# Kernel optimization log

Measured on AMD Instinct MI355X. Metric: run time of the kernel, lower is better.

The kernel has to match this reference:

```python
import jax, jax.numpy as jnp
import numpy as np

D = 2048      # hidden
H = 16        # heads
HD = 128      # head dim
E = 64        # experts
K = 8         # top-k
F = 1024      # expert intermediate
B, S = 1, 256
EPS = 1e-05
THETA = 10000.0
SCALE = 0.08838834764831845  # 1/sqrt(128)


def _rms(x, w):
    return x * jax.lax.rsqrt(jnp.mean(x * x, axis=-1, keepdims=True) + EPS) * w


def _rotate_half(x):
    h = x.shape[-1] // 2
    return jnp.concatenate([-x[..., h:], x[..., :h]], axis=-1)


def setup_inputs() -> dict:
    key = jax.random.key(0)
    ks = jax.random.split(key, 16)
    std = 0.02
    return {
        "x": jax.random.normal(ks[0], (B, S, D), jnp.float32),
        "ln1_w": jnp.ones((D,), jnp.float32),
        "q_w": jax.random.normal(ks[1], (D, D), jnp.float32) * std,
        "k_w": jax.random.normal(ks[2], (D, D), jnp.float32) * std,
        "v_w": jax.random.normal(ks[3], (D, D), jnp.float32) * std,
        "o_w": jax.random.normal(ks[4], (D, D), jnp.float32) * std,
        "qn_w": jnp.ones((D,), jnp.float32),
        "kn_w": jnp.ones((D,), jnp.float32),
        "ln2_w": jnp.ones((D,), jnp.float32),
        "router_w": jax.random.normal(ks[5], (E, D), jnp.float32) * std,
        "gate_w": jax.random.normal(ks[6], (E, F, D), jnp.float32) * std,
        "up_w": jax.random.normal(ks[7], (E, F, D), jnp.float32) * std,
        "down_w": jax.random.normal(ks[8], (E, D, F), jnp.float32) * std,
    }


def reference(x, ln1_w, q_w, k_w, v_w, o_w, qn_w, kn_w, ln2_w,
              router_w, gate_w, up_w, down_w):
    b, s, d = x.shape
    # ---- attention ----
    xn = _rms(x, ln1_w)
    q = _rms(jnp.einsum('bsd,od->bso', xn, q_w), qn_w)
    k = _rms(jnp.einsum('bsd,od->bso', xn, k_w), kn_w)
    v = jnp.einsum('bsd,od->bso', xn, v_w)
    q = q.reshape(b, s, H, HD).transpose(0, 2, 1, 3)  # [b,h,s,hd]
    k = k.reshape(b, s, H, HD).transpose(0, 2, 1, 3)
    v = v.reshape(b, s, H, HD).transpose(0, 2, 1, 3)
    # RoPE
    inv_freq = 1.0 / (THETA ** (jnp.arange(0, HD, 2, dtype=jnp.float32) / HD))
    ang = jnp.arange(s, dtype=jnp.float32)[:, None] * inv_freq[None, :]  # [s, hd/2]
    emb = jnp.concatenate([ang, ang], axis=-1)
    cos, sin = jnp.cos(emb).astype(x.dtype), jnp.sin(emb).astype(x.dtype)
    q = q * cos + _rotate_half(q) * sin
    k = k * cos + _rotate_half(k) * sin
    scores = jnp.einsum('bhqd,bhkd->bhqk', q, k) * SCALE
    causal = jnp.tril(jnp.ones((s, s), bool))
    scores = jnp.where(causal, scores, jnp.finfo(scores.dtype).min)
    attn = jax.nn.softmax(scores, axis=-1)
    ctx = jnp.einsum('bhqk,bhkd->bhqd', attn, v)
    ctx = ctx.transpose(0, 2, 1, 3).reshape(b, s, d)
    h = x + jnp.einsum('bsd,od->bso', ctx, o_w)
    # ---- MoE ----
    hn = _rms(h, ln2_w)
    logits = jnp.einsum('bsd,ed->bse', hn, router_w)
    probs = jax.nn.softmax(logits.astype(jnp.float32), axis=-1)
    vals, idx = jax.lax.top_k(probs, K)  # [b,s,K]
    # dense combine weights [b,s,E]; OLMoE does not renormalize top-k probs
    combine = jnp.sum(jax.nn.one_hot(idx, E, dtype=jnp.float32) * vals[..., None], axis=-2)
    combine = combine.reshape(-1, E).astype(x.dtype)  # [T,E]
    xf = hn.reshape(-1, d)                            # [T,D]
    g = jnp.einsum('td,efd->etf', xf, gate_w)         # [E,T,F]
    u = jnp.einsum('td,efd->etf', xf, up_w)
    mid = jax.nn.silu(g) * u
    eo = jnp.einsum('etf,edf->etd', mid, down_w)      # [E,T,D]
    y = jnp.einsum('te,etd->td', combine, eo).reshape(b, s, d)
    return h + y
```

## Files before the change

kernel.cpp:

```cpp
#include <hip/hip_runtime.h>
#include <math.h>

#define DHID 2048
#define TOK 256
#define NHEAD 16
#define HDIM 128
#define NEXP 64
#define KSEL 8
#define FFD 1024
#define RMSEPS 1e-5f
#define ATTNSCALE 0.08838834764831845f

typedef short bf16x8 __attribute__((ext_vector_type(8)));
typedef float f32x4 __attribute__((ext_vector_type(4)));

__device__ __forceinline__ float bf2f(unsigned short u){
  union { unsigned int u; float f; } c; c.u = ((unsigned int)u)<<16; return c.f;
}
__device__ __forceinline__ unsigned short f2bf(float f){
  union { float f; unsigned int u; } c; c.f = f;
  unsigned int u = c.u + 0x7fffu + ((c.u>>16)&1u);
  return (unsigned short)(u>>16);
}
__device__ __forceinline__ unsigned int pk2(float a, float b){
  return (unsigned int)f2bf(a) | ((unsigned int)f2bf(b)<<16);
}
__device__ __forceinline__ bf16x8 as_bf8(uint4 u){
  union { uint4 u; bf16x8 v; } c; c.u = u; return c.v;
}

#define WAITV(N) { asm volatile("s_waitcnt vmcnt(" #N ")" ::: "memory"); __builtin_amdgcn_sched_barrier(0); }
#define WAITL0   { asm volatile("s_waitcnt lgkmcnt(0)" ::: "memory"); __builtin_amdgcn_sched_barrier(0); }
#define SB       __builtin_amdgcn_sched_barrier(0);

__global__ __launch_bounds__(256) void rms_kernel(const float* __restrict__ x,
    const float* __restrict__ w, unsigned short* __restrict__ obf,
    float* __restrict__ of32)
{
  int row = blockIdx.x, tid = threadIdx.x;
  const float* xr = x + (size_t)row*DHID;
  float4 a = *(const float4*)(xr + tid*8);
  float4 b = *(const float4*)(xr + tid*8 + 4);
  float ss = a.x*a.x+a.y*a.y+a.z*a.z+a.w*a.w + b.x*b.x+b.y*b.y+b.z*b.z+b.w*b.w;
  #pragma unroll
  for(int o=32;o>0;o>>=1) ss += __shfl_down(ss,o);
  __shared__ float red[4];
  if((tid&63)==0) red[tid>>6]=ss;
  __syncthreads();
  float r = rsqrtf((red[0]+red[1]+red[2]+red[3])*(1.0f/DHID) + RMSEPS);
  float v[8] = {a.x,a.y,a.z,a.w,b.x,b.y,b.z,b.w};
  unsigned short ob[8];
  #pragma unroll
  for(int j=0;j<8;j++){
    float val = v[j]*r*w[tid*8+j];
    ob[j]=f2bf(val);
    if(of32) of32[(size_t)row*DHID + tid*8 + j] = val;
  }
  uint4 o4;
  o4.x = (unsigned int)ob[0] | ((unsigned int)ob[1]<<16);
  o4.y = (unsigned int)ob[2] | ((unsigned int)ob[3]<<16);
  o4.z = (unsigned int)ob[4] | ((unsigned int)ob[5]<<16);
  o4.w = (unsigned int)ob[6] | ((unsigned int)ob[7]<<16);
  *(uint4*)(obf + (size_t)row*DHID + tid*8) = o4;
}

__global__ void rope_table_kernel(float* __restrict__ cs, float* __restrict__ sn){
  int i = blockIdx.x*256 + threadIdx.x;
  int s = i>>6, j = i&63;
  float invf = powf(10000.0f, -(float)j*(1.0f/64.0f));
  float ang = (float)s * invf;
  cs[i] = cosf(ang); sn[i] = sinf(ang);
}

__global__ __launch_bounds__(256) void gemm_qkv_kernel(
    const unsigned short* __restrict__ A,
    const float* __restrict__ qw, const float* __restrict__ kw, const float* __restrict__ vw,
    float* __restrict__ qo, float* __restrict__ ko, float* __restrict__ vo)
{
  int nt = blockIdx.x, mt = blockIdx.y;
  int which = nt>>5, nb = nt&31;
  const float* W = (which==0)? qw : (which==1)? kw : vw;
  float* OUT = (which==0)? qo : (which==1)? ko : vo;
  int n0 = nb*64, m0 = mt*64;
  __shared__ unsigned short As[64*64];
  __shared__ unsigned short Bs[64*64];
  int tid = threadIdx.x;
  int wid = tid>>6, lane = tid&63;
  int wm = wid>>1, wn = wid&1;
  int lr = lane&15, lg = lane>>4;
  int sr = tid>>2, sq = tid&3;
  f32x4 acc[2][2] = {};
  const unsigned short* Ap = A + (size_t)(m0+sr)*DHID + sq*16;
  const float* Bp = W + (size_t)(n0+sr)*DHID + sq*16;
  for(int k0=0;k0<DHID;k0+=64){
    uint4 a0 = *(const uint4*)(Ap + k0);
    uint4 a1 = *(const uint4*)(Ap + k0 + 8);
    float4 b0 = *(const float4*)(Bp + k0);
    float4 b1 = *(const float4*)(Bp + k0 + 4);
    float4 b2 = *(const float4*)(Bp + k0 + 8);
    float4 b3 = *(const float4*)(Bp + k0 + 12);
    int x7 = sr&7;
    *(uint4*)&As[sr*64 + (((sq*2)  ^ x7)*8)] = a0;
    *(uint4*)&As[sr*64 + (((sq*2+1)^ x7)*8)] = a1;
    uint4 p0 = make_uint4(pk2(b0.x,b0.y),pk2(b0.z,b0.w),pk2(b1.x,b1.y),pk2(b1.z,b1.w));
    uint4 p1 = make_uint4(pk2(b2.x,b2.y),pk2(b2.z,b2.w),pk2(b3.x,b3.y),pk2(b3.z,b3.w));
    *(uint4*)&Bs[sr*64 + (((sq*2)  ^ x7)*8)] = p0;
    *(uint4*)&Bs[sr*64 + (((sq*2+1)^ x7)*8)] = p1;
    __syncthreads();
    #pragma unroll
    for(int ki=0;ki<2;ki++){
      bf16x8 af[2], bfr[2];
      #pragma unroll
      for(int mi=0;mi<2;mi++){
        int r = wm*32 + mi*16 + lr;
        af[mi] = *(const bf16x8*)&As[r*64 + (((ki*4+lg)^(r&7))*8)];
      }
      #pragma unroll
      for(int ni=0;ni<2;ni++){
        int r = wn*32 + ni*16 + lr;
        bfr[ni] = *(const bf16x8*)&Bs[r*64 + (((ki*4+lg)^(r&7))*8)];
      }
      #pragma unroll
      for(int mi=0;mi<2;mi++)
        #pragma unroll
        for(int ni=0;ni<2;ni++)
          acc[mi][ni] = __builtin_amdgcn_mfma_f32_16x16x32_bf16(af[mi], bfr[ni], acc[mi][ni], 0,0,0);
    }
    __syncthreads();
  }
  #pragma unroll
  for(int mi=0;mi<2;mi++){
    #pragma unroll
    for(int ni=0;ni<2;ni++){
      int col = n0 + wn*32 + ni*16 + lr;
      int rowb = m0 + wm*32 + mi*16 + lg*4;
      #pragma unroll
      for(int rg=0;rg<4;rg++)
        OUT[(size_t)(rowb+rg)*DHID + col] = acc[mi][ni][rg];
    }
  }
}

__global__ __launch_bounds__(256) void gemm_o_kernel(const float* __restrict__ A,
  const float* __restrict__ W, const float* __restrict__ X,
  float* __restrict__ H, float* __restrict__ O)
{
  int nb = blockIdx.x, mt = blockIdx.y;
  int n0 = nb*64, m0 = mt*64;
  __shared__ unsigned short As[64*64];
  __shared__ unsigned short Bs[64*64];
  int tid = threadIdx.x;
  int wid = tid>>6, lane = tid&63;
  int wm = wid>>1, wn = wid&1;
  int lr = lane&15, lg = lane>>4;
  int sr = tid>>2, sq = tid&3;
  f32x4 acc[2][2] = {};
  const float* Ap = A + (size_t)(m0+sr)*DHID + sq*16;
  const float* Bp = W + (size_t)(n0+sr)*DHID + sq*16;
  for(int k0=0;k0<DHID;k0+=64){
    float4 a0=*(const float4*)(Ap+k0),   a1=*(const float4*)(Ap+k0+4);
    float4 a2=*(const float4*)(Ap+k0+8), a3=*(const float4*)(Ap+k0+12);
    float4 b0=*(const float4*)(Bp+k0),   b1=*(const float4*)(Bp+k0+4);
    float4 b2=*(const float4*)(Bp+k0+8), b3=*(const float4*)(Bp+k0+12);
    int x7 = sr&7;
    uint4 pa0 = make_uint4(pk2(a0.x,a0.y),pk2(a0.z,a0.w),pk2(a1.x,a1.y),pk2(a1.z,a1.w));
    uint4 pa1 = make_uint4(pk2(a2.x,a2.y),pk2(a2.z,a2.w),pk2(a3.x,a3.y),pk2(a3.z,a3.w));
    uint4 pb0 = make_uint4(pk2(b0.x,b0.y),pk2(b0.z,b0.w),pk2(b1.x,b1.y),pk2(b1.z,b1.w));
    uint4 pb1 = make_uint4(pk2(b2.x,b2.y),pk2(b2.z,b2.w),pk2(b3.x,b3.y),pk2(b3.z,b3.w));
    *(uint4*)&As[sr*64 + (((sq*2)  ^ x7)*8)] = pa0;
    *(uint4*)&As[sr*64 + (((sq*2+1)^ x7)*8)] = pa1;
    *(uint4*)&Bs[sr*64 + (((sq*2)  ^ x7)*8)] = pb0;
    *(uint4*)&Bs[sr*64 + (((sq*2+1)^ x7)*8)] = pb1;
    __syncthreads();
    #pragma unroll
    for(int ki=0;ki<2;ki++){
      bf16x8 af[2], bfr[2];
      #pragma unroll
      for(int mi=0;mi<2;mi++){
        int r = wm*32 + mi*16 + lr;
        af[mi] = *(const bf16x8*)&As[r*64 + (((ki*4+lg)^(r&7))*8)];
      }
      #pragma unroll
      for(int ni=0;ni<2;ni++){
        int r = wn*32 + ni*16 + lr;
        bfr[ni] = *(const bf16x8*)&Bs[r*64 + (((ki*4+lg)^(r&7))*8)];
      }
      #pragma unroll
      for(int mi=0;mi<2;mi++)
        #pragma unroll
        for(int ni=0;ni<2;ni++)
          acc[mi][ni] = __builtin_amdgcn_mfma_f32_16x16x32_bf16(af[mi], bfr[ni], acc[mi][ni], 0,0,0);
    }
    __syncthreads();
  }
  #pragma unroll
  for(int mi=0;mi<2;mi++){
    #pragma unroll
    for(int ni=0;ni<2;ni++){
      int col = n0 + wn*32 + ni*16 + lr;
      int rowb = m0 + wm*32 + mi*16 + lg*4;
      #pragma unroll
      for(int rg=0;rg<4;rg++){
        size_t idx = (size_t)(rowb+rg)*DHID + col;
        float v = acc[mi][ni][rg] + X[idx];
        H[idx] = v; O[idx] = v;
      }
    }
  }
}

__global__ __launch_bounds__(256) void qknorm_rope_kernel(const float* __restrict__ in,
   const float* __restrict__ w, const float* __restrict__ cs, const float* __restrict__ sn,
   float* __restrict__ out)
{
  int t = blockIdx.x, tid = threadIdx.x;
  __shared__ float xs[DHID];
  const float* xr = in + (size_t)t*DHID;
  float4 a = *(const float4*)(xr + tid*8);
  float4 b = *(const float4*)(xr + tid*8 + 4);
  *(float4*)&xs[tid*8] = a; *(float4*)&xs[tid*8+4] = b;
  float ss = a.x*a.x+a.y*a.y+a.z*a.z+a.w*a.w + b.x*b.x+b.y*b.y+b.z*b.z+b.w*b.w;
  #pragma unroll
  for(int o=32;o>0;o>>=1) ss += __shfl_down(ss,o);
  __shared__ float red[4];
  if((tid&63)==0) red[tid>>6]=ss;
  __syncthreads();
  float r = rsqrtf((red[0]+red[1]+red[2]+red[3])*(1.0f/DHID) + RMSEPS);
  int hh = tid>>4, jb = (tid&15)*4;
  #pragma unroll
  for(int p=0;p<4;p++){
    int j = jb+p;
    int i0 = hh*HDIM + j, i1 = i0+64;
    float va = xs[i0]*r*w[i0];
    float vb = xs[i1]*r*w[i1];
    float c = cs[t*64+j], s = sn[t*64+j];
    out[((size_t)(hh*TOK + t))*HDIM + j]    = va*c - vb*s;
    out[((size_t)(hh*TOK + t))*HDIM + j+64] = vb*c + va*s;
  }
}

__global__ __launch_bounds__(256) void vreshape_kernel(const float* __restrict__ v,
    float* __restrict__ vh)
{
  int t = blockIdx.x, tid = threadIdx.x;
  int i = tid*8;
  int hh = i>>7, d0 = i&127;
  float4 a = *(const float4*)(v + (size_t)t*DHID + i);
  float4 b = *(const float4*)(v + (size_t)t*DHID + i + 4);
  *(float4*)(vh + ((size_t)(hh*TOK+t))*HDIM + d0)     = a;
  *(float4*)(vh + ((size_t)(hh*TOK+t))*HDIM + d0 + 4) = b;
}

__global__ __launch_bounds__(256) void attn_kernel(const float* __restrict__ qh,
  const float* __restrict__ kh, const float* __restrict__ vh, float* __restrict__ ctx)
{
  int head = blockIdx.x>>4, qt = blockIdx.x&15;
  __shared__ float qs[16][132];
  __shared__ float sc[16][260];
  __shared__ float red[16][16];
  __shared__ float rmx[16], rsm[16];
  int tid = threadIdx.x;
  {
    int r = tid>>4, c = (tid&15)*8;
    const float* src = qh + ((size_t)(head*TOK + qt*16 + r))*HDIM + c;
    *(float4*)&qs[r][c]   = *(const float4*)(src);
    *(float4*)&qs[r][c+4] = *(const float4*)(src+4);
  }
  __syncthreads();
  int qi = tid&15, kk = tid>>4;
  int qg = qt*16 + qi;
  for(int k=kk; k<=qg; k+=16){
    const float* kp = kh + ((size_t)(head*TOK + k))*HDIM;
    float d = 0.f;
    #pragma unroll 8
    for(int c=0;c<128;c+=4){
      float4 kv = *(const float4*)(kp + c);
      float4 qv = *(const float4*)&qs[qi][c];
      d += qv.x*kv.x + qv.y*kv.y + qv.z*kv.z + qv.w*kv.w;
    }
    sc[qi][k] = d*ATTNSCALE;
  }
  float m = -1e30f;
  for(int k=kk;k<=qg;k+=16) m = fmaxf(m, sc[qi][k]);
  red[qi][kk] = m;
  __syncthreads();
  if(kk==0){
    float mm=-1e30f;
    #pragma unroll
    for(int j=0;j<16;j++) mm = fmaxf(mm, red[qi][j]);
    rmx[qi]=mm;
  }
  __syncthreads();
  float mm = rmx[qi];
  float s = 0.f;
  for(int k=kk;k<=qg;k+=16){ float pp = expf(sc[qi][k]-mm); sc[qi][k]=pp; s+=pp; }
  red[qi][kk]=s;
  __syncthreads();
  if(kk==0){
    float t_=0.f;
    #pragma unroll
    for(int j=0;j<16;j++) t_ += red[qi][j];
    rsm[qi]=t_;
  }
  __syncthreads();
  int dg = kk;
  float acc[8]={0,0,0,0,0,0,0,0};
  const float* vp = vh + (size_t)head*TOK*HDIM + dg*8;
  for(int k=0;k<=qg;k++){
    float p = sc[qi][k];
    float4 v0 = *(const float4*)(vp + (size_t)k*HDIM);
    float4 v1 = *(const float4*)(vp + (size_t)k*HDIM + 4);
    acc[0]+=p*v0.x; acc[1]+=p*v0.y; acc[2]+=p*v0.z; acc[3]+=p*v0.w;
    acc[4]+=p*v1.x; acc[5]+=p*v1.y; acc[6]+=p*v1.z; acc[7]+=p*v1.w;
  }
  float inv = 1.0f/rsm[qi];
  float* op = ctx + ((size_t)(qt*16+qi))*DHID + head*HDIM + dg*8;
  *(float4*)(op)   = make_float4(acc[0]*inv, acc[1]*inv, acc[2]*inv, acc[3]*inv);
  *(float4*)(op+4) = make_float4(acc[4]*inv, acc[5]*inv, acc[6]*inv, acc[7]*inv);
}

__global__ __launch_bounds__(256) void router_kernel(const float* __restrict__ hn,
    const float* __restrict__ rw, int* __restrict__ counts, int* __restrict__ toklist,
    float* __restrict__ wlist)
{
  int t = blockIdx.x, tid = threadIdx.x;
  __shared__ float xs[DHID];
  __shared__ float part[NEXP*4];
  __shared__ float probs[NEXP];
  *(float4*)&xs[tid*8]   = *(const float4*)(hn + (size_t)t*DHID + tid*8);
  *(float4*)&xs[tid*8+4] = *(const float4*)(hn + (size_t)t*DHID + tid*8+4);
  __syncthreads();
  int e = tid&63, c = tid>>6;
  const float* w = rw + (size_t)e*DHID + c*512;
  const float* xc = xs + c*512;
  float d = 0.f;
  for(int i=0;i<512;i+=4){
    float4 wv = *(const float4*)(w+i);
    d += xc[i]*wv.x + xc[i+1]*wv.y + xc[i+2]*wv.z + xc[i+3]*wv.w;
  }
  part[c*64 + e] = d;
  __syncthreads();
  if(tid<64){
    float logit = part[tid] + part[64+tid] + part[128+tid] + part[192+tid];
    float m = logit;
    #pragma unroll
    for(int o=32;o>0;o>>=1) m = fmaxf(m, __shfl_xor(m,o));
    float p = expf(logit - m);
    float s = p;
    #pragma unroll
    for(int o=32;o>0;o>>=1) s += __shfl_xor(s,o);
    probs[tid] = p/s;
  }
  __syncthreads();
  if(tid==0){
    unsigned long long used = 0ull;
    for(int r=0;r<KSEL;r++){
      float best = -1.f; int bi = 0;
      for(int j=0;j<NEXP;j++){
        if(!((used>>j)&1ull) && probs[j]>best){ best=probs[j]; bi=j; }
      }
      used |= (1ull<<bi);
      int slot = atomicAdd(&counts[bi],1);
      toklist[bi*TOK+slot] = t;
      wlist[bi*TOK+slot] = best;
    }
  }
}

__global__ void scan_kernel(const int* __restrict__ counts, int* __restrict__ offs){
  int e = threadIdx.x;
  int c = counts[e];
  int v = c;
  #pragma unroll
  for(int o=1;o<64;o<<=1){
    int n = __shfl_up(v,o);
    if(e>=o) v += n;
  }
  offs[e] = v - c;
}

__global__ __launch_bounds__(256,4) void moe_gateup_kernel(const unsigned short* __restrict__ hnb,
  const float* __restrict__ gw, const float* __restrict__ uw,
  const int* __restrict__ counts, const int* __restrict__ offs,
  const int* __restrict__ toklist, const float* __restrict__ wlist,
  unsigned short* __restrict__ mid)
{
  int fb = blockIdx.x, e = blockIdx.y, mc = blockIdx.z;
  int cnt = counts[e];
  if(mc*32 >= cnt) return;
  int base = offs[e];
  __shared__ unsigned short Gs[64*64];
  __shared__ unsigned short Us[64*64];
  int tid = threadIdx.x, w = tid>>6, lane = tid&63;
  int wm = w>>1, wn = w&1, lr = lane&15, lg = lane>>4;
  int sr = tid>>2, sq = tid&3, x7 = sr&7;

  const float* Gp = gw + ((size_t)e*FFD + fb*64 + sr)*DHID + sq*16;
  const float* Up = uw + ((size_t)e*FFD + fb*64 + sr)*DHID + sq*16;
  int aslot = mc*32 + wm*16 + lr;
  int acl = (aslot<cnt)? aslot : (cnt-1);
  const unsigned short* Ap = hnb + (size_t)toklist[e*TOK+acl]*DHID + lg*8;

  f32x4 ag[2]={}, au[2]={};
  float4 A_g0,A_g1,A_g2,A_g3, A_u0,A_u1,A_u2,A_u3;
  float4 B_g0,B_g1,B_g2,B_g3, B_u0,B_u1,B_u2,B_u3;
  uint4  A_a0,A_a1, B_a0,B_a1;

  #define GU_ISSUE_W(P,k0) { \
    P##g0=*(const float4*)(Gp+(k0));    P##g1=*(const float4*)(Gp+(k0)+4); \
    P##g2=*(const float4*)(Gp+(k0)+8);  P##g3=*(const float4*)(Gp+(k0)+12); \
    P##u0=*(const float4*)(Up+(k0));    P##u1=*(const float4*)(Up+(k0)+4); \
    P##u2=*(const float4*)(Up+(k0)+8);  P##u3=*(const float4*)(Up+(k0)+12); }
  #define GU_ISSUE_A(P,k0) { \
    P##a0=*(const uint4*)(Ap+(k0)); P##a1=*(const uint4*)(Ap+(k0)+32); }
  #define GU_WRITE(P) { \
    uint4 q0=make_uint4(pk2(P##g0.x,P##g0.y),pk2(P##g0.z,P##g0.w),pk2(P##g1.x,P##g1.y),pk2(P##g1.z,P##g1.w)); \
    uint4 q1=make_uint4(pk2(P##g2.x,P##g2.y),pk2(P##g2.z,P##g2.w),pk2(P##g3.x,P##g3.y),pk2(P##g3.z,P##g3.w)); \
    uint4 q2=make_uint4(pk2(P##u0.x,P##u0.y),pk2(P##u0.z,P##u0.w),pk2(P##u1.x,P##u1.y),pk2(P##u1.z,P##u1.w)); \
    uint4 q3=make_uint4(pk2(P##u2.x,P##u2.y),pk2(P##u2.z,P##u2.w),pk2(P##u3.x,P##u3.y),pk2(P##u3.z,P##u3.w)); \
    *(uint4*)&Gs[sr*64 + (((sq*2)  ^x7)*8)] = q0; \
    *(uint4*)&Gs[sr*64 + (((sq*2+1)^x7)*8)] = q1; \
    *(uint4*)&Us[sr*64 + (((sq*2)  ^x7)*8)] = q2; \
    *(uint4*)&Us[sr*64 + (((sq*2+1)^x7)*8)] = q3; }
  #define GU_COMPUTE(P) { \
    bf16x8 af0=as_bf8(P##a0), af1=as_bf8(P##a1); \
    _Pragma("unroll") \
    for(int ni=0;ni<2;ni++){ \
      int R = wn*32 + ni*16 + lr; \
      _Pragma("unroll") \
      for(int ki=0;ki<2;ki++){ \
        int off = R*64 + (((ki*4+lg)^(R&7))*8); \
        bf16x8 gfr = *(const bf16x8*)&Gs[off]; \
        bf16x8 ufr = *(const bf16x8*)&Us[off]; \
        bf16x8 afk = ki ? af1 : af0; \
        ag[ni] = __builtin_amdgcn_mfma_f32_16x16x32_bf16(afk, gfr, ag[ni], 0,0,0); \
        au[ni] = __builtin_amdgcn_mfma_f32_16x16x32_bf16(afk, ufr, au[ni], 0,0,0); \
      } \
    } }

  const int NT = DHID/64;
  GU_ISSUE_W(A_,0)   GU_ISSUE_A(A_,0)
  GU_ISSUE_W(B_,64)  GU_ISSUE_A(B_,64)

  for(int t=0;t<NT;t+=2){
    WAITV(10)
    GU_WRITE(A_)
    if(t+2<NT){ GU_ISSUE_W(A_,(t+2)*64) }
    WAITL0
    __builtin_amdgcn_s_barrier(); SB
    GU_COMPUTE(A_)
    if(t+2<NT){ GU_ISSUE_A(A_,(t+2)*64) }
    __builtin_amdgcn_s_barrier(); SB
    if(t+3<NT){ WAITV(10) } else { WAITV(0) }
    GU_WRITE(B_)
    if(t+3<NT){ GU_ISSUE_W(B_,(t+3)*64) }
    WAITL0
    __builtin_amdgcn_s_barrier(); SB
    GU_COMPUTE(B_)
    if(t+3<NT){ GU_ISSUE_A(B_,(t+3)*64) }
    __builtin_amdgcn_s_barrier(); SB
  }
  #undef GU_ISSUE_W
  #undef GU_ISSUE_A
  #undef GU_WRITE
  #undef GU_COMPUTE

  #pragma unroll
  for(int ni=0;ni<2;ni++){
    int f = fb*64 + wn*32 + ni*16 + lr;
    #pragma unroll
    for(int rg=0;rg<4;rg++){
      int sl = wm*16 + lg*4 + rg;
      int slot = mc*32 + sl;
      if(slot < cnt){
        float cw = wlist[e*TOK + slot];
        float g = ag[ni][rg], u = au[ni][rg];
        float mval = g/(1.0f+expf(-g))*u*cw;
        mid[((size_t)(base+slot))*FFD + f] = f2bf(mval);
      }
    }
  }
}

__global__ __launch_bounds__(256,4) void moe_down_kernel(const unsigned short* __restrict__ mid,
  const float* __restrict__ dwn, const int* __restrict__ counts, const int* __restrict__ offs,
  const int* __restrict__ toklist, float* __restrict__ out)
{
  int nb=blockIdx.x, e=blockIdx.y, mc=blockIdx.z;
  int cnt=counts[e];
  if(mc*32>=cnt) return;
  int base=offs[e];
  __shared__ unsigned short Ds[64*64];
  int tid=threadIdx.x, w=tid>>6, lane=tid&63;
  int wm=w>>1, wn=w&1, lr=lane&15, lg=lane>>4;
  int sr=tid>>2, sq=tid&3, x7=sr&7;

  const float* Dp = dwn + ((size_t)e*DHID + nb*64 + sr)*FFD + sq*16;
  int slot0 = mc*32 + wm*16 + lr;
  int sla = (slot0<cnt)? slot0 : (cnt-1);
  const unsigned short* Ap = mid + (size_t)(base+sla)*FFD + lg*8;

  f32x4 acc[2]={};
  float4 A_d0,A_d1,A_d2,A_d3, B_d0,B_d1,B_d2,B_d3;
  uint4  A_a0,A_a1, B_a0,B_a1;

  #define D_ISSUE_W(P,k0) { \
    P##d0=*(const float4*)(Dp+(k0));    P##d1=*(const float4*)(Dp+(k0)+4); \
    P##d2=*(const float4*)(Dp+(k0)+8);  P##d3=*(const float4*)(Dp+(k0)+12); }
  #define D_ISSUE_A(P,k0) { \
    P##a0=*(const uint4*)(Ap+(k0)); P##a1=*(const uint4*)(Ap+(k0)+32); }
  #define D_WRITE(P) { \
    uint4 q0=make_uint4(pk2(P##d0.x,P##d0.y),pk2(P##d0.z,P##d0.w),pk2(P##d1.x,P##d1.y),pk2(P##d1.z,P##d1.w)); \
    uint4 q1=make_uint4(pk2(P##d2.x,P##d2.y),pk2(P##d2.z,P##d2.w),pk2(P##d3.x,P##d3.y),pk2(P##d3.z,P##d3.w)); \
    *(uint4*)&Ds[sr*64 + (((sq*2)  ^x7)*8)] = q0; \
    *(uint4*)&Ds[sr*64 + (((sq*2+1)^x7)*8)] = q1; }
  #define D_COMPUTE(P) { \
    bf16x8 af0=as_bf8(P##a0), af1=as_bf8(P##a1); \
    _Pragma("unroll") \
    for(int ni=0;ni<2;ni++){ \
      int R = wn*32 + ni*16 + lr; \
      _Pragma("unroll") \
      for(int ki=0;ki<2;ki++){ \
        int off = R*64 + (((ki*4+lg)^(R&7))*8); \
        bf16x8 dfr = *(const bf16x8*)&Ds[off]; \
        bf16x8 afk = ki ? af1 : af0; \
        acc[ni] = __builtin_amdgcn_mfma_f32_16x16x32_bf16(afk, dfr, acc[ni], 0,0,0); \
      } \
    } }

  const int NT = FFD/64;
  D_ISSUE_W(A_,0)   D_ISSUE_A(A_,0)
  D_ISSUE_W(B_,64)  D_ISSUE_A(B_,64)

  for(int t=0;t<NT;t+=2){
    WAITV(6)
    D_WRITE(A_)
    if(t+2<NT){ D_ISSUE_W(A_,(t+2)*64) }
    WAITL0
    __builtin_amdgcn_s_barrier(); SB
    D_COMPUTE(A_)
    if(t+2<NT){ D_ISSUE_A(A_,(t+2)*64) }
    __builtin_amdgcn_s_barrier(); SB
    if(t+3<NT){ WAITV(6) } else { WAITV(0) }
    D_WRITE(B_)
    if(t+3<NT){ D_ISSUE_W(B_,(t+3)*64) }
    WAITL0
    __builtin_amdgcn_s_barrier(); SB
    D_COMPUTE(B_)
    if(t+3<NT){ D_ISSUE_A(B_,(t+3)*64) }
    __builtin_amdgcn_s_barrier(); SB
  }
  #undef D_ISSUE_W
  #undef D_ISSUE_A
  #undef D_WRITE
  #undef D_COMPUTE

  #pragma unroll
  for(int ni=0;ni<2;ni++){
    int d = nb*64 + wn*32 + ni*16 + lr;
    #pragma unroll
    for(int rg=0;rg<4;rg++){
      int sl=wm*16+lg*4+rg, slot=mc*32+sl;
      if(slot<cnt){
        int tok = toklist[e*TOK + slot];
        atomicAdd(out + (size_t)tok*DHID + d, acc[ni][rg]);
      }
    }
  }
}

extern "C" void kernel_launch(void* const* d_in, const int* in_sizes, int n_in,
                              void* d_out, int out_size, void* d_ws, size_t ws_size,
                              hipStream_t stream)
{
  (void)in_sizes; (void)n_in; (void)out_size; (void)ws_size;
  const float* x    = (const float*)d_in[0];
  const float* ln1w = (const float*)d_in[1];
  const float* qw   = (const float*)d_in[2];
  const float* kw   = (const float*)d_in[3];
  const float* vw   = (const float*)d_in[4];
  const float* ow   = (const float*)d_in[5];
  const float* qnw  = (const float*)d_in[6];
  const float* knw  = (const float*)d_in[7];
  const float* ln2w = (const float*)d_in[8];
  const float* rw   = (const float*)d_in[9];
  const float* gw   = (const float*)d_in[10];
  const float* uw   = (const float*)d_in[11];
  const float* dwn  = (const float*)d_in[12];
  float* out = (float*)d_out;

  char* p = (char*)d_ws;
  auto alloc = [&](size_t bytes)->void*{ void* r = (void*)p; p += (bytes + 255) & ~(size_t)255; return r; };
  unsigned short* xnb = (unsigned short*)alloc((size_t)TOK*DHID*2);
  float* qf   = (float*)alloc((size_t)TOK*DHID*4);
  float* kf   = (float*)alloc((size_t)TOK*DHID*4);
  float* vf   = (float*)alloc((size_t)TOK*DHID*4);
  float* qh   = (float*)alloc((size_t)TOK*DHID*4);
  float* kh   = (float*)alloc((size_t)TOK*DHID*4);
  float* vh   = (float*)alloc((size_t)TOK*DHID*4);
  float* ctx  = (float*)alloc((size_t)TOK*DHID*4);
  float* hbuf = (float*)alloc((size_t)TOK*DHID*4);
  float* hnf  = (float*)alloc((size_t)TOK*DHID*4);
  unsigned short* hnb = (unsigned short*)alloc((size_t)TOK*DHID*2);
  float* csb  = (float*)alloc((size_t)TOK*64*4);
  float* snb  = (float*)alloc((size_t)TOK*64*4);
  int* counts = (int*)alloc(NEXP*4);
  int* offs   = (int*)alloc(NEXP*4);
  int* toklist= (int*)alloc((size_t)NEXP*TOK*4);
  float* wlist= (float*)alloc((size_t)NEXP*TOK*4);
  unsigned short* mid = (unsigned short*)alloc((size_t)TOK*KSEL*FFD*2);

  rope_table_kernel<<<64,256,0,stream>>>(csb,snb);
  rms_kernel<<<TOK,256,0,stream>>>(x, ln1w, xnb, nullptr);
  gemm_qkv_kernel<<<dim3(96,4),256,0,stream>>>(xnb,qw,kw,vw,qf,kf,vf);
  qknorm_rope_kernel<<<TOK,256,0,stream>>>(qf,qnw,csb,snb,qh);
  qknorm_rope_kernel<<<TOK,256,0,stream>>>(kf,knw,csb,snb,kh);
  vreshape_kernel<<<TOK,256,0,stream>>>(vf,vh);
  attn_kernel<<<256,256,0,stream>>>(qh,kh,vh,ctx);
  gemm_o_kernel<<<dim3(32,4),256,0,stream>>>(ctx,ow,x,hbuf,out);
  rms_kernel<<<TOK,256,0,stream>>>(hbuf, ln2w, hnb, hnf);
  hipMemsetAsync(counts,0,NEXP*4,stream);
  router_kernel<<<TOK,256,0,stream>>>(hnf,rw,counts,toklist,wlist);
  scan_kernel<<<1,64,0,stream>>>(counts,offs);
  moe_gateup_kernel<<<dim3(16,NEXP,8),256,0,stream>>>(hnb,gw,uw,counts,offs,toklist,wlist,mid);
  moe_down_kernel<<<dim3(32,NEXP,8),256,0,stream>>>(mid,dwn,counts,offs,toklist,out);
}
```

Baseline: 707.5 us.

## Widen MoE K-tiles to 256 with coalesced weight loads; drop V reshape kernel

The MoE gate/up and down kernels now stage 256-wide K slices of the fp32 expert weights into LDS per step instead of 64-wide ones. Each thread issues eight strided float4 loads per half-tile, so adjacent lanes read adjacent 16-byte chunks and coalescing improves. Barriers per K step are also fewer. The cost is a much larger LDS footprint and register count, and launch bounds drop to 2 and 3 blocks per CU, so occupancy falls. Separately, the attention kernel reads V directly from the token-major projection output, which removes the vreshape kernel launch and its copy.

Result: faster. 642.2 us (-9.2%).

```diff
diff --git a/kernel.cpp b/kernel.cpp
--- a/kernel.cpp
+++ b/kernel.cpp
@@ -14,9 +14,6 @@
 typedef short bf16x8 __attribute__((ext_vector_type(8)));
 typedef float f32x4 __attribute__((ext_vector_type(4)));
 
-__device__ __forceinline__ float bf2f(unsigned short u){
-  union { unsigned int u; float f; } c; c.u = ((unsigned int)u)<<16; return c.f;
-}
 __device__ __forceinline__ unsigned short f2bf(float f){
   union { float f; unsigned int u; } c; c.f = f;
   unsigned int u = c.u + 0x7fffu + ((c.u>>16)&1u);
@@ -239,20 +236,8 @@
   }
 }
 
-__global__ __launch_bounds__(256) void vreshape_kernel(const float* __restrict__ v,
-    float* __restrict__ vh)
-{
-  int t = blockIdx.x, tid = threadIdx.x;
-  int i = tid*8;
-  int hh = i>>7, d0 = i&127;
-  float4 a = *(const float4*)(v + (size_t)t*DHID + i);
-  float4 b = *(const float4*)(v + (size_t)t*DHID + i + 4);
-  *(float4*)(vh + ((size_t)(hh*TOK+t))*HDIM + d0)     = a;
-  *(float4*)(vh + ((size_t)(hh*TOK+t))*HDIM + d0 + 4) = b;
-}
-
 __global__ __launch_bounds__(256) void attn_kernel(const float* __restrict__ qh,
-  const float* __restrict__ kh, const float* __restrict__ vh, float* __restrict__ ctx)
+  const float* __restrict__ kh, const float* __restrict__ vf, float* __restrict__ ctx)
 {
   int head = blockIdx.x>>4, qt = blockIdx.x&15;
   __shared__ float qs[16][132];
@@ -305,11 +290,11 @@
   __syncthreads();
   int dg = kk;
   float acc[8]={0,0,0,0,0,0,0,0};
-  const float* vp = vh + (size_t)head*TOK*HDIM + dg*8;
+  const float* vp = vf + head*HDIM + dg*8;
   for(int k=0;k<=qg;k++){
     float p = sc[qi][k];
-    float4 v0 = *(const float4*)(vp + (size_t)k*HDIM);
-    float4 v1 = *(const float4*)(vp + (size_t)k*HDIM + 4);
+    float4 v0 = *(const float4*)(vp + (size_t)k*DHID);
+    float4 v1 = *(const float4*)(vp + (size_t)k*DHID + 4);
     acc[0]+=p*v0.x; acc[1]+=p*v0.y; acc[2]+=p*v0.z; acc[3]+=p*v0.w;
     acc[4]+=p*v1.x; acc[5]+=p*v1.y; acc[6]+=p*v1.z; acc[7]+=p*v1.w;
   }
@@ -379,7 +364,7 @@
   offs[e] = v - c;
 }
 
-__global__ __launch_bounds__(256,4) void moe_gateup_kernel(const unsigned short* __restrict__ hnb,
+__global__ __launch_bounds__(256,2) void moe_gateup_kernel(const unsigned short* __restrict__ hnb,
   const float* __restrict__ gw, const float* __restrict__ uw,
   const int* __restrict__ counts, const int* __restrict__ offs,
   const int* __restrict__ toklist, const float* __restrict__ wlist,
@@ -389,81 +374,80 @@
   int cnt = counts[e];
   if(mc*32 >= cnt) return;
   int base = offs[e];
-  __shared__ unsigned short Gs[64*64];
-  __shared__ unsigned short Us[64*64];
+  __shared__ unsigned short Gs[64*256];
+  __shared__ unsigned short Us[64*256];
   int tid = threadIdx.x, w = tid>>6, lane = tid&63;
   int wm = w>>1, wn = w&1, lr = lane&15, lg = lane>>4;
-  int sr = tid>>2, sq = tid&3, x7 = sr&7;
-
-  const float* Gp = gw + ((size_t)e*FFD + fb*64 + sr)*DHID + sq*16;
-  const float* Up = uw + ((size_t)e*FFD + fb*64 + sr)*DHID + sq*16;
+  int srow = tid>>2, sc4 = tid&3, rx = srow&7;
+  int halfo = (sc4&1)*4, vbase = sc4>>1;
+
+  const float* Gp = gw + ((size_t)e*FFD + fb*64 + srow)*DHID + sc4*4;
+  const float* Up = uw + ((size_t)e*FFD + fb*64 + srow)*DHID + sc4*4;
   int aslot = mc*32 + wm*16 + lr;
   int acl = (aslot<cnt)? aslot : (cnt-1);
   const unsigned short* Ap = hnb + (size_t)toklist[e*TOK+acl]*DHID + lg*8;
 
   f32x4 ag[2]={}, au[2]={};
-  float4 A_g0,A_g1,A_g2,A_g3, A_u0,A_u1,A_u2,A_u3;
-  float4 B_g0,B_g1,B_g2,B_g3, B_u0,B_u1,B_u2,B_u3;
-  uint4  A_a0,A_a1, B_a0,B_a1;
-
-  #define GU_ISSUE_W(P,k0) { \
-    P##g0=*(const float4*)(Gp+(k0));    P##g1=*(const float4*)(Gp+(k0)+4); \
-    P##g2=*(const float4*)(Gp+(k0)+8);  P##g3=*(const float4*)(Gp+(k0)+12); \
-    P##u0=*(const float4*)(Up+(k0));    P##u1=*(const float4*)(Up+(k0)+4); \
-    P##u2=*(const float4*)(Up+(k0)+8);  P##u3=*(const float4*)(Up+(k0)+12); }
-  #define GU_ISSUE_A(P,k0) { \
-    P##a0=*(const uint4*)(Ap+(k0)); P##a1=*(const uint4*)(Ap+(k0)+32); }
-  #define GU_WRITE(P) { \
-    uint4 q0=make_uint4(pk2(P##g0.x,P##g0.y),pk2(P##g0.z,P##g0.w),pk2(P##g1.x,P##g1.y),pk2(P##g1.z,P##g1.w)); \
-    uint4 q1=make_uint4(pk2(P##g2.x,P##g2.y),pk2(P##g2.z,P##g2.w),pk2(P##g3.x,P##g3.y),pk2(P##g3.z,P##g3.w)); \
-    uint4 q2=make_uint4(pk2(P##u0.x,P##u0.y),pk2(P##u0.z,P##u0.w),pk2(P##u1.x,P##u1.y),pk2(P##u1.z,P##u1.w)); \
-    uint4 q3=make_uint4(pk2(P##u2.x,P##u2.y),pk2(P##u2.z,P##u2.w),pk2(P##u3.x,P##u3.y),pk2(P##u3.z,P##u3.w)); \
-    *(uint4*)&Gs[sr*64 + (((sq*2)  ^x7)*8)] = q0; \
-    *(uint4*)&Gs[sr*64 + (((sq*2+1)^x7)*8)] = q1; \
-    *(uint4*)&Us[sr*64 + (((sq*2)  ^x7)*8)] = q2; \
-    *(uint4*)&Us[sr*64 + (((sq*2+1)^x7)*8)] = q3; }
-  #define GU_COMPUTE(P) { \
-    bf16x8 af0=as_bf8(P##a0), af1=as_bf8(P##a1); \
-    _Pragma("unroll") \
-    for(int ni=0;ni<2;ni++){ \
-      int R = wn*32 + ni*16 + lr; \
+  float4 P[8], Q[8];
+  uint4 av[8];
+
+  #define ISSUE(BK,SRC,s,jb) { \
+    _Pragma("unroll") \
+    for(int j=0;j<8;j++) BK[j] = *(const float4*)(SRC + (s)*256 + ((jb)+j)*16); }
+  #define WRITE(BK,DST,jb) { \
+    _Pragma("unroll") \
+    for(int j=0;j<8;j++){ \
+      int v = ((jb)+j)*2 + vbase; \
+      int vp = (v & ~7) | ((v&7) ^ rx); \
+      uint2 val; val.x = pk2(BK[j].x,BK[j].y); val.y = pk2(BK[j].z,BK[j].w); \
+      *(uint2*)&DST[srow*256 + vp*8 + halfo] = val; } }
+  #define ISSUE_A(s) { \
+    _Pragma("unroll") \
+    for(int kf=0;kf<8;kf++) av[kf] = *(const uint4*)(Ap + (s)*256 + kf*32); }
+  #define COMPUTE() { \
+    _Pragma("unroll") \
+    for(int kf=0;kf<8;kf++){ \
+      bf16x8 af = as_bf8(av[kf]); \
       _Pragma("unroll") \
-      for(int ki=0;ki<2;ki++){ \
-        int off = R*64 + (((ki*4+lg)^(R&7))*8); \
-        bf16x8 gfr = *(const bf16x8*)&Gs[off]; \
-        bf16x8 ufr = *(const bf16x8*)&Us[off]; \
-        bf16x8 afk = ki ? af1 : af0; \
-        ag[ni] = __builtin_amdgcn_mfma_f32_16x16x32_bf16(afk, gfr, ag[ni], 0,0,0); \
-        au[ni] = __builtin_amdgcn_mfma_f32_16x16x32_bf16(afk, ufr, au[ni], 0,0,0); \
+      for(int ni=0;ni<2;ni++){ \
+        int R = wn*32 + ni*16 + lr; \
+        int v = kf*4 + lg; \
+        int vp = (v & ~7) | ((v&7) ^ (lr&7)); \
+        int ho = R*256 + vp*8; \
+        bf16x8 gfr = *(const bf16x8*)&Gs[ho]; \
+        bf16x8 ufr = *(const bf16x8*)&Us[ho]; \
+        ag[ni] = __builtin_amdgcn_mfma_f32_16x16x32_bf16(af, gfr, ag[ni], 0,0,0); \
+        au[ni] = __builtin_amdgcn_mfma_f32_16x16x32_bf16(af, ufr, au[ni], 0,0,0); \
       } \
     } }
 
-  const int NT = DHID/64;
-  GU_ISSUE_W(A_,0)   GU_ISSUE_A(A_,0)
-  GU_ISSUE_W(B_,64)  GU_ISSUE_A(B_,64)
-
-  for(int t=0;t<NT;t+=2){
-    WAITV(10)
-    GU_WRITE(A_)
-    if(t+2<NT){ GU_ISSUE_W(A_,(t+2)*64) }
+  const int NS = DHID/256;
+  ISSUE(P, Gp, 0, 0)
+  ISSUE(Q, Gp, 0, 8)
+  for(int s=0;s<NS;s++){
+    WAITV(8)
+    WRITE(P, Gs, 0)
+    ISSUE(P, Up, s, 0)
+    WAITV(8)
+    WRITE(Q, Gs, 8)
+    ISSUE(Q, Up, s, 8)
+    WAITV(8)
+    WRITE(P, Us, 0)
+    ISSUE_A(s)
+    WAITV(8)
+    WRITE(Q, Us, 8)
+    if(s+1<NS){ ISSUE(P, Gp, s+1, 0) }
     WAITL0
     __builtin_amdgcn_s_barrier(); SB
-    GU_COMPUTE(A_)
-    if(t+2<NT){ GU_ISSUE_A(A_,(t+2)*64) }
+    if(s+1<NS){ WAITV(8) } else { WAITV(0) }
+    COMPUTE()
+    if(s+1<NS){ ISSUE(Q, Gp, s+1, 8) }
     __builtin_amdgcn_s_barrier(); SB
-    if(t+3<NT){ WAITV(10) } else { WAITV(0) }
-    GU_WRITE(B_)
-    if(t+3<NT){ GU_ISSUE_W(B_,(t+3)*64) }
-    WAITL0
-    __builtin_amdgcn_s_barrier(); SB
-    GU_COMPUTE(B_)
-    if(t+3<NT){ GU_ISSUE_A(B_,(t+3)*64) }
-    __builtin_amdgcn_s_barrier(); SB
-  }
-  #undef GU_ISSUE_W
-  #undef GU_ISSUE_A
-  #undef GU_WRITE
-  #undef GU_COMPUTE
+  }
+  #undef ISSUE
+  #undef WRITE
+  #undef ISSUE_A
+  #undef COMPUTE
 
   #pragma unroll
   for(int ni=0;ni<2;ni++){
@@ -482,7 +466,7 @@
   }
 }
 
-__global__ __launch_bounds__(256,4) void moe_down_kernel(const unsigned short* __restrict__ mid,
+__global__ __launch_bounds__(256,3) void moe_down_kernel(const unsigned short* __restrict__ mid,
   const float* __restrict__ dwn, const int* __restrict__ counts, const int* __restrict__ offs,
   const int* __restrict__ toklist, float* __restrict__ out)
 {
@@ -490,70 +474,69 @@
   int cnt=counts[e];
   if(mc*32>=cnt) return;
   int base=offs[e];
-  __shared__ unsigned short Ds[64*64];
+  __shared__ unsigned short Ds[64*256];
   int tid=threadIdx.x, w=tid>>6, lane=tid&63;
   int wm=w>>1, wn=w&1, lr=lane&15, lg=lane>>4;
-  int sr=tid>>2, sq=tid&3, x7=sr&7;
-
-  const float* Dp = dwn + ((size_t)e*DHID + nb*64 + sr)*FFD + sq*16;
+  int srow=tid>>2, sc4=tid&3, rx=srow&7;
+  int halfo=(sc4&1)*4, vbase=sc4>>1;
+
+  const float* Dp = dwn + ((size_t)e*DHID + nb*64 + srow)*FFD + sc4*4;
   int slot0 = mc*32 + wm*16 + lr;
   int sla = (slot0<cnt)? slot0 : (cnt-1);
   const unsigned short* Ap = mid + (size_t)(base+sla)*FFD + lg*8;
 
   f32x4 acc[2]={};
-  float4 A_d0,A_d1,A_d2,A_d3, B_d0,B_d1,B_d2,B_d3;
-  uint4  A_a0,A_a1, B_a0,B_a1;
-
-  #define D_ISSUE_W(P,k0) { \
-    P##d0=*(const float4*)(Dp+(k0));    P##d1=*(const float4*)(Dp+(k0)+4); \
-    P##d2=*(const float4*)(Dp+(k0)+8);  P##d3=*(const float4*)(Dp+(k0)+12); }
-  #define D_ISSUE_A(P,k0) { \
-    P##a0=*(const uint4*)(Ap+(k0)); P##a1=*(const uint4*)(Ap+(k0)+32); }
-  #define D_WRITE(P) { \
-    uint4 q0=make_uint4(pk2(P##d0.x,P##d0.y),pk2(P##d0.z,P##d0.w),pk2(P##d1.x,P##d1.y),pk2(P##d1.z,P##d1.w)); \
-    uint4 q1=make_uint4(pk2(P##d2.x,P##d2.y),pk2(P##d2.z,P##d2.w),pk2(P##d3.x,P##d3.y),pk2(P##d3.z,P##d3.w)); \
-    *(uint4*)&Ds[sr*64 + (((sq*2)  ^x7)*8)] = q0; \
-    *(uint4*)&Ds[sr*64 + (((sq*2+1)^x7)*8)] = q1; }
-  #define D_COMPUTE(P) { \
-    bf16x8 af0=as_bf8(P##a0), af1=as_bf8(P##a1); \
-    _Pragma("unroll") \
-    for(int ni=0;ni<2;ni++){ \
-      int R = wn*32 + ni*16 + lr; \
+  float4 P[8], Q[8];
+  uint4 av[8];
+
+  #define ISSUE(BK,s,jb) { \
+    _Pragma("unroll") \
+    for(int j=0;j<8;j++) BK[j] = *(const float4*)(Dp + (s)*256 + ((jb)+j)*16); }
+  #define WRITE(BK,jb) { \
+    _Pragma("unroll") \
+    for(int j=0;j<8;j++){ \
+      int v = ((jb)+j)*2 + vbase; \
+      int vp = (v & ~7) | ((v&7) ^ rx); \
+      uint2 val; val.x = pk2(BK[j].x,BK[j].y); val.y = pk2(BK[j].z,BK[j].w); \
+      *(uint2*)&Ds[srow*256 + vp*8 + halfo] = val; } }
+  #define ISSUE_A(s) { \
+    _Pragma("unroll") \
+    for(int kf=0;kf<8;kf++) av[kf] = *(const uint4*)(Ap + (s)*256 + kf*32); }
+  #define COMPUTE() { \
+    _Pragma("unroll") \
+    for(int kf=0;kf<8;kf++){ \
+      bf16x8 af = as_bf8(av[kf]); \
       _Pragma("unroll") \
-      for(int ki=0;ki<2;ki++){ \
-        int off = R*64 + (((ki*4+lg)^(R&7))*8); \
-        bf16x8 dfr = *(const bf16x8*)&Ds[off]; \
-        bf16x8 afk = ki ? af1 : af0; \
-        acc[ni] = __builtin_amdgcn_mfma_f32_16x16x32_bf16(afk, dfr, acc[ni], 0,0,0); \
+      for(int ni=0;ni<2;ni++){ \
+        int R = wn*32 + ni*16 + lr; \
+        int v = kf*4 + lg; \
+        int vp = (v & ~7) | ((v&7) ^ (lr&7)); \
+        bf16x8 dfr = *(const bf16x8*)&Ds[R*256 + vp*8]; \
+        acc[ni] = __builtin_amdgcn_mfma_f32_16x16x32_bf16(af, dfr, acc[ni], 0,0,0); \
       } \
     } }
 
-  const int NT = FFD/64;
-  D_ISSUE_W(A_,0)   D_ISSUE_A(A_,0)
-  D_ISSUE_W(B_,64)  D_ISSUE_A(B_,64)
-
-  for(int t=0;t<NT;t+=2){
-    WAITV(6)
-    D_WRITE(A_)
-    if(t+2<NT){ D_ISSUE_W(A_,(t+2)*64) }
+  const int NS = FFD/256;
+  ISSUE(P, 0, 0)
+  ISSUE(Q, 0, 8)
+  for(int s=0;s<NS;s++){
+    WAITV(8)
+    WRITE(P, 0)
+    ISSUE_A(s)
+    WAITV(8)
+    WRITE(Q, 8)
+    if(s+1<NS){ ISSUE(P, s+1, 0) }
     WAITL0
     __builtin_amdgcn_s_barrier(); SB
-    D_COMPUTE(A_)
-    if(t+2<NT){ D_ISSUE_A(A_,(t+2)*64) }
+    if(s+1<NS){ WAITV(8) } else { WAITV(0) }
+    COMPUTE()
+    if(s+1<NS){ ISSUE(Q, s+1, 8) }
     __builtin_amdgcn_s_barrier(); SB
-    if(t+3<NT){ WAITV(6) } else { WAITV(0) }
-    D_WRITE(B_)
-    if(t+3<NT){ D_ISSUE_W(B_,(t+3)*64) }
-    WAITL0
-    __builtin_amdgcn_s_barrier(); SB
-    D_COMPUTE(B_)
-    if(t+3<NT){ D_ISSUE_A(B_,(t+3)*64) }
-    __builtin_amdgcn_s_barrier(); SB
-  }
-  #undef D_ISSUE_W
-  #undef D_ISSUE_A
-  #undef D_WRITE
-  #undef D_COMPUTE
+  }
+  #undef ISSUE
+  #undef WRITE
+  #undef ISSUE_A
+  #undef COMPUTE
 
   #pragma unroll
   for(int ni=0;ni<2;ni++){
@@ -597,7 +580,6 @@
   float* vf   = (float*)alloc((size_t)TOK*DHID*4);
   float* qh   = (float*)alloc((size_t)TOK*DHID*4);
   float* kh   = (float*)alloc((size_t)TOK*DHID*4);
-  float* vh   = (float*)alloc((size_t)TOK*DHID*4);
   float* ctx  = (float*)alloc((size_t)TOK*DHID*4);
   float* hbuf = (float*)alloc((size_t)TOK*DHID*4);
   float* hnf  = (float*)alloc((size_t)TOK*DHID*4);
@@ -615,8 +597,7 @@
   gemm_qkv_kernel<<<dim3(96,4),256,0,stream>>>(xnb,qw,kw,vw,qf,kf,vf);
   qknorm_rope_kernel<<<TOK,256,0,stream>>>(qf,qnw,csb,snb,qh);
   qknorm_rope_kernel<<<TOK,256,0,stream>>>(kf,knw,csb,snb,kh);
-  vreshape_kernel<<<TOK,256,0,stream>>>(vf,vh);
-  attn_kernel<<<256,256,0,stream>>>(qh,kh,vh,ctx);
+  attn_kernel<<<256,256,0,stream>>>(qh,kh,vf,ctx);
   gemm_o_kernel<<<dim3(32,4),256,0,stream>>>(ctx,ow,x,hbuf,out);
   rms_kernel<<<TOK,256,0,stream>>>(hbuf, ln2w, hnb, hnf);
   hipMemsetAsync(counts,0,NEXP*4,stream);
```
